# Performance work log

Hardware: AMD Instinct MI355X
Metric: run time of the kernel (lower is better)

The kernel has to match this reference:

```python
import jax, jax.numpy as jnp
import numpy as np

EMBED_DIM = 1024
NUM_HEADS = 16
HEAD_DIM = EMBED_DIM // NUM_HEADS
B, S = 2, 2048


def setup_inputs() -> dict:
    key = jax.random.key(0)
    ks = jax.random.split(key, 8)
    std = 1.0 / np.sqrt(EMBED_DIM)
    return {
        "xq": jax.random.normal(ks[0], (B, S, EMBED_DIM), jnp.float32),
        "xk": jax.random.normal(ks[1], (B, S, EMBED_DIM), jnp.float32),
        "xv": jax.random.normal(ks[2], (B, S, EMBED_DIM), jnp.float32),
        "Wq": jax.random.normal(ks[3], (EMBED_DIM, EMBED_DIM), jnp.float32) * std,
        "Wk": jax.random.normal(ks[4], (EMBED_DIM, EMBED_DIM), jnp.float32) * std,
        "Wv": jax.random.normal(ks[5], (EMBED_DIM, EMBED_DIM), jnp.float32) * std,
        "Wo": jax.random.normal(ks[6], (EMBED_DIM, EMBED_DIM), jnp.float32) * std,
        "bo": jnp.zeros((EMBED_DIM,), jnp.float32),
    }


def reference(xq, xk, xv, Wq, Wk, Wv, Wo, bo):
    # nn.Linear(x) = x @ W.T ; then view last dim into (heads, head_dim)
    def proj(x, W):
        y = jnp.einsum('bse,fe->bsf', x, W)
        return y.reshape(x.shape[0], x.shape[1], NUM_HEADS, HEAD_DIM)

    q = proj(xq, Wq)  # [b, m, h, f]
    k = proj(xk, Wk)  # [b, n, h, f]
    v = proj(xv, Wv)  # [b, n, h, f]

    scaling = 1.0 / np.sqrt(HEAD_DIM).astype(np.float32)
    dot = scaling * jnp.einsum('bmhf,bnhf->bhmn', q, k)  # [b, h, m, n]
    attn = jax.nn.softmax(dot, axis=-1)
    out = jnp.einsum('bhmn,bnhf->bmhf', attn, v)  # [b, m, h, f]

    Wo_hf = Wo.reshape(EMBED_DIM, NUM_HEADS, HEAD_DIM)
    return jnp.einsum('bmhf,ehf->bme', out, Wo_hf) + bo
```

## Files before the change

### kernel.cpp

```cpp
#include <hip/hip_runtime.h>
#include <math.h>


#define EMBED 1024
#define SEQ   2048
#define BATCH 2
#define NH    16
#define HD    64

typedef __attribute__((ext_vector_type(8))) short bf16x8;
typedef __attribute__((ext_vector_type(4))) short bf16x4;
typedef __attribute__((ext_vector_type(4))) float f32x4;
typedef __attribute__((ext_vector_type(4))) unsigned int u32x4;

#define QSCALE 0.18033688f

__device__ inline unsigned short f2bf(float f) {
  unsigned int u = __builtin_bit_cast(unsigned int, f);
  u += 0x7fffu + ((u >> 16) & 1u);
  return (unsigned short)(u >> 16);
}
__device__ inline float bf2f(unsigned short s) {
  unsigned int u = ((unsigned int)s) << 16;
  return __builtin_bit_cast(float, u);
}

__device__ inline unsigned packbf(float lo, float hi) {
  return __builtin_amdgcn_perm(__builtin_bit_cast(unsigned int, hi),
                               __builtin_bit_cast(unsigned int, lo),
                               0x07060302u);
}

__device__ inline void async_cp16(const void* g, void* l) {
  __builtin_amdgcn_global_load_lds(
      (const __attribute__((address_space(1))) unsigned int*)g,
      (__attribute__((address_space(3))) unsigned int*)l, 16, 0, 0);
}

__global__ void detect_kernel(const unsigned int* __restrict__ xq, int* __restrict__ flag) {
  __shared__ int cnt[256];
  int t = threadIdx.x;
  unsigned int w = xq[t];
  unsigned int e = (w >> 7) & 0xFFu;
  cnt[t] = (e >= 0x70u && e <= 0x8Fu) ? 1 : 0;
  __syncthreads();
  for (int s = 128; s > 0; s >>= 1) {
    if (t < s) cnt[t] += cnt[t + s];
    __syncthreads();
  }
  if (t == 0) *flag = (cnt[0] >= 160) ? 1 : 0;
}

struct PackPtrs {
  const void* src[7];
  unsigned short* dst[7];
};
__global__ __launch_bounds__(256) void pack_all(PackPtrs p, const int* __restrict__ flagp) {
  const bool isbf = (*flagp != 0);
  int ci = blockIdx.x * 256 + threadIdx.x;
  int t, rel;
  if (ci < 1572864) { t = ci / 524288; rel = ci - t * 524288; }
  else { int r = ci - 1572864; int w = r / 131072; t = 3 + w; rel = r - w * 131072; }
  size_t off = (size_t)rel * 8;
  unsigned short* d = p.dst[t] + off;
  if (isbf) {
    *(bf16x8*)d = *(const bf16x8*)((const unsigned short*)p.src[t] + off);
  } else {
    const float* s = (const float*)p.src[t] + off;
    f32x4 f0 = *(const f32x4*)s;
    f32x4 f1 = *(const f32x4*)(s + 4);
    bf16x8 v;
#pragma unroll
    for (int e = 0; e < 4; ++e) {
      v[e] = (short)f2bf(f0[e]);
      v[4 + e] = (short)f2bf(f1[e]);
    }
    *(bf16x8*)d = v;
  }
}

struct QkvArgs {
  const unsigned short* A[3];
  const unsigned short* W[3];
  unsigned short* out[3];
};
__global__ __launch_bounds__(256) void gemm_qkv(QkvArgs args) {
  __shared__ __align__(16) unsigned short smem[16640];

  const int z = blockIdx.z;
  const unsigned short* A = args.A[z];
  const unsigned short* Bw = args.W[z];
  unsigned short* out = args.out[z];

  const int tid = threadIdx.x, lane = tid & 63, wave = tid >> 6;
  const int wm = wave >> 1, wn = wave & 1;
  const int q = lane >> 4, c = lane & 15;
  const int m0 = blockIdx.x * 128, n0 = blockIdx.y * 128;

  f32x4 acc[4][4];
#pragma unroll
  for (int i = 0; i < 4; ++i)
#pragma unroll
    for (int j = 0; j < 4; ++j) acc[i][j] = (f32x4){0.f, 0.f, 0.f, 0.f};

  auto STAGE = [&](int buf, int k0) {
#pragma unroll
    for (int jj = 0; jj < 2; ++jj) {
      int ci = jj * 256 + tid;
      async_cp16(A + (size_t)(m0 + (ci >> 2)) * EMBED + k0 + (ci & 3) * 8,
                 (void*)(smem + buf * 8192 + (jj * 256 + wave * 64) * 8));
      async_cp16(Bw + (size_t)(n0 + (ci >> 2)) * EMBED + k0 + (ci & 3) * 8,
                 (void*)(smem + buf * 8192 + 4096 + (jj * 256 + wave * 64) * 8));
    }
  };

  STAGE(0, 0);
  __syncthreads();
  for (int kt = 0; kt < EMBED / 32; ++kt) {
    const int p = kt & 1;
    if (kt + 1 < EMBED / 32) STAGE(1 - p, (kt + 1) * 32);
    const unsigned short* Ab = smem + p * 8192;
    const unsigned short* Bb = smem + p * 8192 + 4096;

    bf16x8 af[4], bfr[4];
#pragma unroll
    for (int i = 0; i < 4; ++i)
      af[i] = *(const bf16x8*)(Ab + (wm * 64 + i * 16 + c) * 32 + q * 8);
#pragma unroll
    for (int j = 0; j < 4; ++j)
      bfr[j] = *(const bf16x8*)(Bb + (wn * 64 + j * 16 + c) * 32 + q * 8);
#pragma unroll
    for (int i = 0; i < 4; ++i)
#pragma unroll
      for (int j = 0; j < 4; ++j)
        acc[i][j] = __builtin_amdgcn_mfma_f32_16x16x32_bf16(af[i], bfr[j], acc[i][j], 0, 0, 0);
    __syncthreads();
  }

  if (z < 2) {
    const float sc = (z == 0) ? QSCALE : 1.0f;
#pragma unroll
    for (int i = 0; i < 4; ++i)
#pragma unroll
      for (int j = 0; j < 4; ++j)
#pragma unroll
        for (int r = 0; r < 4; ++r) {
          int m = m0 + wm * 64 + i * 16 + q * 4 + r;
          int col = n0 + wn * 64 + j * 16 + c;
          int b = m >> 11, s = m & 2047, h = col >> 6, d = col & 63;
          out[(size_t)((b * NH + h) * SEQ + s) * HD + d] = f2bf(acc[i][j][r] * sc);
        }
  } else {
    __syncthreads();
#pragma unroll
    for (int i = 0; i < 4; ++i)
#pragma unroll
      for (int j = 0; j < 4; ++j)
#pragma unroll
        for (int r = 0; r < 4; ++r)
          smem[(wm * 64 + i * 16 + q * 4 + r) * 130 + wn * 64 + j * 16 + c] =
              f2bf(acc[i][j][r]);
    __syncthreads();
    int n = tid >> 1;
    int sh = (tid & 1) * 64;
    int b = m0 >> 11, s0l = m0 & 2047;
    int h = blockIdx.y * 2 + (n >> 6), d = n & 63;
    unsigned short* dst = out + (size_t)((b * NH + h) * HD + d) * SEQ + s0l + sh;
#pragma unroll
    for (int g = 0; g < 8; ++g) {
      bf16x8 v;
#pragma unroll
      for (int e = 0; e < 8; ++e) v[e] = (short)smem[(sh + g * 8 + e) * 130 + n];
      *(bf16x8*)(dst + g * 8) = v;
    }
  }
}

__global__ __launch_bounds__(256) void gemm_out(
    const unsigned short* __restrict__ A,
    const unsigned short* __restrict__ Bw,
    const void* __restrict__ bias,
    void* __restrict__ out,
    const int* __restrict__ flagp)
{
  __shared__ __align__(16) unsigned short smem[16384];

  const int tid = threadIdx.x, lane = tid & 63, wave = tid >> 6;
  const int wm = wave >> 1, wn = wave & 1;
  const int q = lane >> 4, c = lane & 15;
  const int m0 = blockIdx.x * 128, n0 = blockIdx.y * 128;

  f32x4 acc[4][4];
#pragma unroll
  for (int i = 0; i < 4; ++i)
#pragma unroll
    for (int j = 0; j < 4; ++j) acc[i][j] = (f32x4){0.f, 0.f, 0.f, 0.f};

  auto STAGE = [&](int buf, int k0) {
#pragma unroll
    for (int jj = 0; jj < 2; ++jj) {
      int ci = jj * 256 + tid;
      async_cp16(A + (size_t)(m0 + (ci >> 2)) * EMBED + k0 + (ci & 3) * 8,
                 (void*)(smem + buf * 8192 + (jj * 256 + wave * 64) * 8));
      async_cp16(Bw + (size_t)(n0 + (ci >> 2)) * EMBED + k0 + (ci & 3) * 8,
                 (void*)(smem + buf * 8192 + 4096 + (jj * 256 + wave * 64) * 8));
    }
  };

  STAGE(0, 0);
  __syncthreads();
  for (int kt = 0; kt < EMBED / 32; ++kt) {
    const int p = kt & 1;
    if (kt + 1 < EMBED / 32) STAGE(1 - p, (kt + 1) * 32);
    const unsigned short* Ab = smem + p * 8192;
    const unsigned short* Bb = smem + p * 8192 + 4096;

    bf16x8 af[4], bfr[4];
#pragma unroll
    for (int i = 0; i < 4; ++i)
      af[i] = *(const bf16x8*)(Ab + (wm * 64 + i * 16 + c) * 32 + q * 8);
#pragma unroll
    for (int j = 0; j < 4; ++j)
      bfr[j] = *(const bf16x8*)(Bb + (wn * 64 + j * 16 + c) * 32 + q * 8);
#pragma unroll
    for (int i = 0; i < 4; ++i)
#pragma unroll
      for (int j = 0; j < 4; ++j)
        acc[i][j] = __builtin_amdgcn_mfma_f32_16x16x32_bf16(af[i], bfr[j], acc[i][j], 0, 0, 0);
    __syncthreads();
  }

  const bool isbf = (*flagp != 0);
#pragma unroll
  for (int i = 0; i < 4; ++i)
#pragma unroll
    for (int j = 0; j < 4; ++j)
#pragma unroll
      for (int r = 0; r < 4; ++r) {
        int m = m0 + wm * 64 + i * 16 + q * 4 + r;
        int col = n0 + wn * 64 + j * 16 + c;
        float v = acc[i][j][r];
        v += isbf ? bf2f(((const unsigned short*)bias)[col]) : ((const float*)bias)[col];
        if (isnan(v)) v = 777.0f;
        if (isbf) ((unsigned short*)out)[(size_t)m * EMBED + col] = f2bf(v);
        else      ((float*)out)[(size_t)m * EMBED + col] = v;
      }
}

__global__ __launch_bounds__(256) void attn_kernel(
    const unsigned short* __restrict__ Qb,
    const unsigned short* __restrict__ Kb,
    const unsigned short* __restrict__ Vtb,
    unsigned short* __restrict__ Ob)
{
  __shared__ __align__(16) unsigned short Kt[2][64][72];
  __shared__ __align__(16) unsigned short Vs[2][64][72];

  const int tid = threadIdx.x;
  const int lane = tid & 63;
  const int wave = tid >> 6;
  const int q = lane >> 4, c = lane & 15;
  const int b = blockIdx.z, h = blockIdx.y;
  const int q0 = blockIdx.x * 128 + wave * 32;

  const unsigned short* Qh = Qb + ((size_t)(b * NH + h) * SEQ) * HD;
  const unsigned short* Kh = Kb + ((size_t)(b * NH + h) * SEQ) * HD;
  const unsigned short* Vh = Vtb + ((size_t)(b * NH + h) * HD) * SEQ;

  bf16x8 qflA = *(const bf16x8*)(Qh + (q0 + c) * HD + q * 8);
  bf16x8 qfhA = *(const bf16x8*)(Qh + (q0 + c) * HD + 32 + q * 8);
  bf16x8 qflB = *(const bf16x8*)(Qh + (q0 + 16 + c) * HD + q * 8);
  bf16x8 qfhB = *(const bf16x8*)(Qh + (q0 + 16 + c) * HD + 32 + q * 8);

  f32x4 oA[4], oB[4];
#pragma unroll
  for (int t = 0; t < 4; ++t) { oA[t] = (f32x4){0.f,0.f,0.f,0.f}; oB[t] = (f32x4){0.f,0.f,0.f,0.f}; }
  f32x4 lA = (f32x4){0.f,0.f,0.f,0.f}, lB = (f32x4){0.f,0.f,0.f,0.f};

  bf16x8 ones;
#pragma unroll
  for (int e = 0; e < 8; ++e) ones[e] = (short)0x3F80;

  const int r0 = tid >> 3;
  const int t7 = tid & 7;
  const int ch0 = t7 * 8;
  const int u0 = 8 * (t7 >> 2) + 4 * (t7 & 1) + ((t7 >> 1) & 1);

  const bf16x8* pK0 = (const bf16x8*)(Kh + (size_t)r0 * HD + ch0);
  const bf16x8* pK1 = (const bf16x8*)(Kh + (size_t)(32 + r0) * HD + ch0);
  const bf16x8* pV0 = (const bf16x8*)(Vh + (size_t)r0 * SEQ + ch0);
  const bf16x8* pV1 = (const bf16x8*)(Vh + (size_t)(32 + r0) * SEQ + ch0);

  bf16x8 kr0, kr1, vr0, vr1;
  kr0 = *pK0; pK0 += (64 * HD) / 8;
  kr1 = *pK1; pK1 += (64 * HD) / 8;
  vr0 = *pV0; pV0 += 64 / 8;
  vr1 = *pV1; pV1 += 64 / 8;
  *(bf16x8*)(&Kt[0][r0][ch0]) = kr0;
  *(bf16x8*)(&Kt[0][32 + r0][ch0]) = kr1;
  {
    bf16x4 lo0 = __builtin_shufflevector(vr0, vr0, 0, 1, 2, 3);
    bf16x4 hi0 = __builtin_shufflevector(vr0, vr0, 4, 5, 6, 7);
    bf16x4 lo1 = __builtin_shufflevector(vr1, vr1, 0, 1, 2, 3);
    bf16x4 hi1 = __builtin_shufflevector(vr1, vr1, 4, 5, 6, 7);
    *(bf16x4*)(&Vs[0][r0][u0 * 4]) = lo0;
    *(bf16x4*)(&Vs[0][r0][u0 * 4 + 8]) = hi0;
    *(bf16x4*)(&Vs[0][32 + r0][u0 * 4]) = lo1;
    *(bf16x4*)(&Vs[0][32 + r0][u0 * 4 + 8]) = hi1;
  }

  for (int kt = 0; kt < SEQ / 64; ++kt) {
    const int p = kt & 1;
    __syncthreads();
    if (kt + 1 < SEQ / 64) {
      kr0 = *pK0; pK0 += (64 * HD) / 8;
      kr1 = *pK1; pK1 += (64 * HD) / 8;
      vr0 = *pV0; pV0 += 64 / 8;
      vr1 = *pV1; pV1 += 64 / 8;
    }

    bf16x8 kf0[4], kf1[4];
#pragma unroll
    for (int s = 0; s < 4; ++s) {
      kf0[s] = *(const bf16x8*)(&Kt[p][s * 16 + c][q * 8]);
      kf1[s] = *(const bf16x8*)(&Kt[p][s * 16 + c][32 + q * 8]);
    }

#pragma unroll
    for (int g = 0; g < 2; ++g) {
      u32x4 pa, pb;
#pragma unroll
      for (int s2 = 0; s2 < 2; ++s2) {
        const int s = g * 2 + s2;
        f32x4 zA = {0.f, 0.f, 0.f, 0.f};
        f32x4 zB = {0.f, 0.f, 0.f, 0.f};
        zA = __builtin_amdgcn_mfma_f32_16x16x32_bf16(kf0[s], qflA, zA, 0, 0, 0);
        zA = __builtin_amdgcn_mfma_f32_16x16x32_bf16(kf1[s], qfhA, zA, 0, 0, 0);
        zB = __builtin_amdgcn_mfma_f32_16x16x32_bf16(kf0[s], qflB, zB, 0, 0, 0);
        zB = __builtin_amdgcn_mfma_f32_16x16x32_bf16(kf1[s], qfhB, zB, 0, 0, 0);
        float a0 = __builtin_amdgcn_exp2f(zA[0]);
        float a1 = __builtin_amdgcn_exp2f(zA[1]);
        float a2 = __builtin_amdgcn_exp2f(zA[2]);
        float a3 = __builtin_amdgcn_exp2f(zA[3]);
        float b0 = __builtin_amdgcn_exp2f(zB[0]);
        float b1 = __builtin_amdgcn_exp2f(zB[1]);
        float b2 = __builtin_amdgcn_exp2f(zB[2]);
        float b3 = __builtin_amdgcn_exp2f(zB[3]);
        pa[s2 * 2]     = packbf(a0, a1);
        pa[s2 * 2 + 1] = packbf(a2, a3);
        pb[s2 * 2]     = packbf(b0, b1);
        pb[s2 * 2 + 1] = packbf(b2, b3);
      }
      bf16x8 pfA = __builtin_bit_cast(bf16x8, pa);
      bf16x8 pfB = __builtin_bit_cast(bf16x8, pb);
      __builtin_amdgcn_s_setprio(1);
      lA = __builtin_amdgcn_mfma_f32_16x16x32_bf16(pfA, ones, lA, 0, 0, 0);
      lB = __builtin_amdgcn_mfma_f32_16x16x32_bf16(pfB, ones, lB, 0, 0, 0);
#pragma unroll
      for (int t = 0; t < 4; ++t) {
        bf16x8 vf = *(const bf16x8*)(&Vs[p][t * 16 + c][(g * 4 + q) * 8]);
        oA[t] = __builtin_amdgcn_mfma_f32_16x16x32_bf16(pfA, vf, oA[t], 0, 0, 0);
        oB[t] = __builtin_amdgcn_mfma_f32_16x16x32_bf16(pfB, vf, oB[t], 0, 0, 0);
      }
      __builtin_amdgcn_s_setprio(0);
    }

    if (kt + 1 < SEQ / 64) {
      *(bf16x8*)(&Kt[1 - p][r0][ch0]) = kr0;
      *(bf16x8*)(&Kt[1 - p][32 + r0][ch0]) = kr1;
      bf16x4 lo0 = __builtin_shufflevector(vr0, vr0, 0, 1, 2, 3);
      bf16x4 hi0 = __builtin_shufflevector(vr0, vr0, 4, 5, 6, 7);
      bf16x4 lo1 = __builtin_shufflevector(vr1, vr1, 0, 1, 2, 3);
      bf16x4 hi1 = __builtin_shufflevector(vr1, vr1, 4, 5, 6, 7);
      *(bf16x4*)(&Vs[1 - p][r0][u0 * 4]) = lo0;
      *(bf16x4*)(&Vs[1 - p][r0][u0 * 4 + 8]) = hi0;
      *(bf16x4*)(&Vs[1 - p][32 + r0][u0 * 4]) = lo1;
      *(bf16x4*)(&Vs[1 - p][32 + r0][u0 * 4 + 8]) = hi1;
    }
  }

  float invA[4], invB[4];
#pragma unroll
  for (int r = 0; r < 4; ++r) { invA[r] = 1.0f / lA[r]; invB[r] = 1.0f / lB[r]; }
#pragma unroll
  for (int t = 0; t < 4; ++t)
#pragma unroll
    for (int r = 0; r < 4; ++r) {
      int col = h * HD + t * 16 + c;
      int srowA = q0 + q * 4 + r;
      float vA = oA[t][r] * invA[r];
      if (isnan(vA)) vA = 77.0f;
      Ob[((size_t)(b * SEQ + srowA)) * EMBED + col] = f2bf(vA);
      int srowB = q0 + 16 + q * 4 + r;
      float vB = oB[t][r] * invB[r];
      if (isnan(vB)) vB = 77.0f;
      Ob[((size_t)(b * SEQ + srowB)) * EMBED + col] = f2bf(vB);
    }
}

__device__ inline bf16x8 load8(const void* p, int idx, bool isbf) {
  if (isbf) return *(const bf16x8*)((const unsigned short*)p + idx);
  const float* f = (const float*)p + idx;
  bf16x8 r;
#pragma unroll
  for (int i = 0; i < 8; ++i) r[i] = (short)f2bf(f[i]);
  return r;
}
__global__ __launch_bounds__(256) void gemm_bt(
    const void* __restrict__ A, const void* __restrict__ Bw,
    const void* __restrict__ bias, void* __restrict__ out,
    const int* __restrict__ flagp, int mode, float scale)
{
  const bool isbf = (*flagp != 0);
  const bool a_isbf = isbf || (mode == 0);
  const int lane = threadIdx.x & 63;
  const int wave = threadIdx.x >> 6;
  const int tile = blockIdx.x * 4 + wave;
  const int mt = tile >> 4, nt = tile & 15;
  const int q = lane >> 4, c = lane & 15;
  const int m0 = mt * 16, n0 = nt * 64;

  f32x4 acc[4];
#pragma unroll
  for (int t = 0; t < 4; ++t) acc[t] = (f32x4){0.f, 0.f, 0.f, 0.f};

  for (int k0 = 0; k0 < EMBED; k0 += 32) {
    bf16x8 a = load8(A, (m0 + c) * EMBED + k0 + q * 8, a_isbf);
#pragma unroll
    for (int t = 0; t < 4; ++t) {
      bf16x8 b = load8(Bw, (n0 + t * 16 + c) * EMBED + k0 + q * 8, isbf);
      acc[t] = __builtin_amdgcn_mfma_f32_16x16x32_bf16(a, b, acc[t], 0, 0, 0);
    }
  }
#pragma unroll
  for (int t = 0; t < 4; ++t)
#pragma unroll
    for (int r = 0; r < 4; ++r) {
      float v = acc[t][r] * scale;
      int row = m0 + q * 4 + r, col = n0 + t * 16 + c;
      if (mode == 0) {
        v += isbf ? bf2f(((const unsigned short*)bias)[col]) : ((const float*)bias)[col];
        if (isbf) ((unsigned short*)out)[row * EMBED + col] = f2bf(v);
        else      ((float*)out)[row * EMBED + col] = v;
      } else {
        int b = row >> 11, s = row & 2047, h = col >> 6, d = col & 63;
        if (mode == 1) ((unsigned short*)out)[(((b * NH + h) * SEQ) + s) * HD + d] = f2bf(v);
        else           ((unsigned short*)out)[(((b * NH + h) * HD) + d) * SEQ + s] = f2bf(v);
      }
    }
}

extern "C" void kernel_launch(void* const* d_in, const int* in_sizes, int n_in,
                              void* d_out, int out_size, void* d_ws, size_t ws_size,
                              hipStream_t stream) {
  const void* xq = d_in[0]; const void* xk = d_in[1]; const void* xv = d_in[2];
  const void* Wq = d_in[3]; const void* Wk = d_in[4]; const void* Wv = d_in[5];
  const void* Wo = d_in[6]; const void* bo = d_in[7];

  const size_t NEL = (size_t)BATCH * SEQ * EMBED;
  const size_t WEL = (size_t)EMBED * EMBED;
  unsigned short* base = (unsigned short*)d_ws;

  unsigned short* Xq = base;
  unsigned short* Xk = Xq + NEL;
  unsigned short* Xv = Xk + NEL;
  unsigned short* Wqb = Xv + NEL;
  unsigned short* Wkb = Wqb + WEL;
  unsigned short* Wvb = Wkb + WEL;
  unsigned short* Wob = Wvb + WEL;
  unsigned short* Q  = Wob + WEL;
  unsigned short* K  = Q + NEL;
  unsigned short* Vt = K + NEL;
  unsigned short* AO = Xq;
  int* flagF = (int*)(Vt + NEL);
  size_t need = ((char*)(flagF + 16)) - (char*)d_ws;

  if (ws_size >= need) {
    detect_kernel<<<1, 256, 0, stream>>>((const unsigned int*)xq, flagF);
    PackPtrs pp;
    pp.src[0] = xq; pp.src[1] = xk; pp.src[2] = xv;
    pp.src[3] = Wq; pp.src[4] = Wk; pp.src[5] = Wv; pp.src[6] = Wo;
    pp.dst[0] = Xq; pp.dst[1] = Xk; pp.dst[2] = Xv;
    pp.dst[3] = Wqb; pp.dst[4] = Wkb; pp.dst[5] = Wvb; pp.dst[6] = Wob;
    pack_all<<<8192, 256, 0, stream>>>(pp, flagF);

    QkvArgs qa;
    qa.A[0] = Xq; qa.A[1] = Xk; qa.A[2] = Xv;
    qa.W[0] = Wqb; qa.W[1] = Wkb; qa.W[2] = Wvb;
    qa.out[0] = Q; qa.out[1] = K; qa.out[2] = Vt;
    gemm_qkv<<<dim3(32, 8, 3), 256, 0, stream>>>(qa);
    attn_kernel<<<dim3(SEQ / 128, NH, BATCH), 256, 0, stream>>>(Q, K, Vt, AO);
    gemm_out<<<dim3(32, 8), 256, 0, stream>>>(AO, Wob, bo, d_out, flagF);
  } else {
    unsigned short* Qf  = base;
    unsigned short* Kf  = Qf + NEL;
    unsigned short* Vtf = Kf + NEL;
    unsigned short* AOf = Vtf + NEL;
    int* flag = (int*)(AOf + NEL);
    detect_kernel<<<1, 256, 0, stream>>>((const unsigned int*)xq, flag);
    dim3 gblk(1024, 1, 1);
    gemm_bt<<<gblk, 256, 0, stream>>>(xq, Wq, nullptr, Qf, flag, 1, QSCALE);
    gemm_bt<<<gblk, 256, 0, stream>>>(xk, Wk, nullptr, Kf, flag, 1, 1.0f);
    gemm_bt<<<gblk, 256, 0, stream>>>(xv, Wv, nullptr, Vtf, flag, 2, 1.0f);
    attn_kernel<<<dim3(SEQ / 128, NH, BATCH), 256, 0, stream>>>(Qf, Kf, Vtf, AOf);
    gemm_bt<<<gblk, 256, 0, stream>>>(AOf, Wo, bo, d_out, flag, 0, 1.0f);
  }
}
```

Baseline: 230.5 us.

## Fuse fp32-to-bf16 conversion into GEMM loads and drop separate pack/detect kernels

Removes the standalone detect and pack_all kernels. The QKV and output GEMMs now load fp32 (or bf16) operands directly from global memory into registers, convert them to bf16, and write them to shared memory in a register-staged double-buffer pipeline. The dtype sniff is recomputed per block inside gemm_qkv. This avoids a full extra read/write pass over the inputs and weights plus two launches, but gives up async global-to-LDS copies and adds conversion ALU work and register pressure in the GEMM main loop.

```diff
diff --git a/kernel.cpp b/kernel.cpp
--- a/kernel.cpp
+++ b/kernel.cpp
@@ -29,12 +29,6 @@
   return __builtin_amdgcn_perm(__builtin_bit_cast(unsigned int, hi),
                                __builtin_bit_cast(unsigned int, lo),
                                0x07060302u);
-}
-
-__device__ inline void async_cp16(const void* g, void* l) {
-  __builtin_amdgcn_global_load_lds(
-      (const __attribute__((address_space(1))) unsigned int*)g,
-      (__attribute__((address_space(3))) unsigned int*)l, 16, 0, 0);
 }
 
 __global__ void detect_kernel(const unsigned int* __restrict__ xq, int* __restrict__ flag) {
@@ -51,45 +45,19 @@
   if (t == 0) *flag = (cnt[0] >= 160) ? 1 : 0;
 }
 
-struct PackPtrs {
-  const void* src[7];
-  unsigned short* dst[7];
-};
-__global__ __launch_bounds__(256) void pack_all(PackPtrs p, const int* __restrict__ flagp) {
-  const bool isbf = (*flagp != 0);
-  int ci = blockIdx.x * 256 + threadIdx.x;
-  int t, rel;
-  if (ci < 1572864) { t = ci / 524288; rel = ci - t * 524288; }
-  else { int r = ci - 1572864; int w = r / 131072; t = 3 + w; rel = r - w * 131072; }
-  size_t off = (size_t)rel * 8;
-  unsigned short* d = p.dst[t] + off;
-  if (isbf) {
-    *(bf16x8*)d = *(const bf16x8*)((const unsigned short*)p.src[t] + off);
-  } else {
-    const float* s = (const float*)p.src[t] + off;
-    f32x4 f0 = *(const f32x4*)s;
-    f32x4 f1 = *(const f32x4*)(s + 4);
-    bf16x8 v;
-#pragma unroll
-    for (int e = 0; e < 4; ++e) {
-      v[e] = (short)f2bf(f0[e]);
-      v[4 + e] = (short)f2bf(f1[e]);
-    }
-    *(bf16x8*)d = v;
-  }
-}
-
 struct QkvArgs {
-  const unsigned short* A[3];
-  const unsigned short* W[3];
+  const void* A[3];
+  const void* W[3];
   unsigned short* out[3];
+  const unsigned int* sniff;
+  int* flag;
 };
 __global__ __launch_bounds__(256) void gemm_qkv(QkvArgs args) {
   __shared__ __align__(16) unsigned short smem[16640];
 
   const int z = blockIdx.z;
-  const unsigned short* A = args.A[z];
-  const unsigned short* Bw = args.W[z];
+  const void* A = args.A[z];
+  const void* Bw = args.W[z];
   unsigned short* out = args.out[z];
 
   const int tid = threadIdx.x, lane = tid & 63, wave = tid >> 6;
@@ -97,30 +65,87 @@
   const int q = lane >> 4, c = lane & 15;
   const int m0 = blockIdx.x * 128, n0 = blockIdx.y * 128;
 
+  int* cnt = (int*)smem;
+  {
+    unsigned int w = args.sniff[tid];
+    unsigned int e = (w >> 7) & 0xFFu;
+    cnt[tid] = (e >= 0x70u && e <= 0x8Fu) ? 1 : 0;
+  }
+  __syncthreads();
+  for (int s = 128; s > 0; s >>= 1) {
+    if (tid < s) cnt[tid] += cnt[tid + s];
+    __syncthreads();
+  }
+  const bool isbf = (cnt[0] >= 160);
+  if (z == 0 && blockIdx.x == 0 && blockIdx.y == 0 && tid == 0)
+    *args.flag = isbf ? 1 : 0;
+  __syncthreads();
+
   f32x4 acc[4][4];
 #pragma unroll
   for (int i = 0; i < 4; ++i)
 #pragma unroll
     for (int j = 0; j < 4; ++j) acc[i][j] = (f32x4){0.f, 0.f, 0.f, 0.f};
 
-  auto STAGE = [&](int buf, int k0) {
-#pragma unroll
-    for (int jj = 0; jj < 2; ++jj) {
-      int ci = jj * 256 + tid;
-      async_cp16(A + (size_t)(m0 + (ci >> 2)) * EMBED + k0 + (ci & 3) * 8,
-                 (void*)(smem + buf * 8192 + (jj * 256 + wave * 64) * 8));
-      async_cp16(Bw + (size_t)(n0 + (ci >> 2)) * EMBED + k0 + (ci & 3) * 8,
-                 (void*)(smem + buf * 8192 + 4096 + (jj * 256 + wave * 64) * 8));
+  f32x4 rf[8];
+  bf16x8 rb[4];
+
+  auto LOAD = [&](int k0) {
+    if (isbf) {
+#pragma unroll
+      for (int j = 0; j < 2; ++j) {
+        int ci2 = j * 256 + tid;
+        rb[j]     = *(const bf16x8*)((const unsigned short*)A +
+                      (size_t)(m0 + (ci2 >> 2)) * EMBED + k0 + (ci2 & 3) * 8);
+        rb[2 + j] = *(const bf16x8*)((const unsigned short*)Bw +
+                      (size_t)(n0 + (ci2 >> 2)) * EMBED + k0 + (ci2 & 3) * 8);
+      }
+    } else {
+#pragma unroll
+      for (int j = 0; j < 2; ++j) {
+        int ci2 = j * 256 + tid;
+        const float* a = (const float*)A + (size_t)(m0 + (ci2 >> 2)) * EMBED + k0 + (ci2 & 3) * 8;
+        const float* b = (const float*)Bw + (size_t)(n0 + (ci2 >> 2)) * EMBED + k0 + (ci2 & 3) * 8;
+        rf[j * 2]     = *(const f32x4*)a;
+        rf[j * 2 + 1] = *(const f32x4*)(a + 4);
+        rf[4 + j * 2]     = *(const f32x4*)b;
+        rf[4 + j * 2 + 1] = *(const f32x4*)(b + 4);
+      }
     }
   };
-
-  STAGE(0, 0);
+  auto CVTWRITE = [&](int buf) {
+#pragma unroll
+    for (int j = 0; j < 2; ++j) {
+      int ci2 = j * 256 + tid;
+      unsigned short* dA = smem + buf * 8192 + ci2 * 8;
+      unsigned short* dB = smem + buf * 8192 + 4096 + ci2 * 8;
+      if (isbf) {
+        *(bf16x8*)dA = rb[j];
+        *(bf16x8*)dB = rb[2 + j];
+      } else {
+        bf16x8 va, vb;
+#pragma unroll
+        for (int e = 0; e < 4; ++e) {
+          va[e]     = (short)f2bf(rf[j * 2][e]);
+          va[4 + e] = (short)f2bf(rf[j * 2 + 1][e]);
+          vb[e]     = (short)f2bf(rf[4 + j * 2][e]);
+          vb[4 + e] = (short)f2bf(rf[4 + j * 2 + 1][e]);
+        }
+        *(bf16x8*)dA = va;
+        *(bf16x8*)dB = vb;
+      }
+    }
+  };
+
+  LOAD(0);
+  CVTWRITE(0);
+  LOAD(32);
   __syncthreads();
+
   for (int kt = 0; kt < EMBED / 32; ++kt) {
     const int p = kt & 1;
-    if (kt + 1 < EMBED / 32) STAGE(1 - p, (kt + 1) * 32);
     const unsigned short* Ab = smem + p * 8192;
-    const unsigned short* Bb = smem + p * 8192 + 4096;
+    const unsigned short* Bb = Ab + 4096;
 
     bf16x8 af[4], bfr[4];
 #pragma unroll
@@ -134,6 +159,9 @@
 #pragma unroll
       for (int j = 0; j < 4; ++j)
         acc[i][j] = __builtin_amdgcn_mfma_f32_16x16x32_bf16(af[i], bfr[j], acc[i][j], 0, 0, 0);
+
+    if (kt + 1 < EMBED / 32) CVTWRITE(1 - p);
+    if (kt + 2 < EMBED / 32) LOAD((kt + 2) * 32);
     __syncthreads();
   }
 
@@ -178,7 +206,7 @@
 
 __global__ __launch_bounds__(256) void gemm_out(
     const unsigned short* __restrict__ A,
-    const unsigned short* __restrict__ Bw,
+    const void* __restrict__ Bw,
     const void* __restrict__ bias,
     void* __restrict__ out,
     const int* __restrict__ flagp)
@@ -190,30 +218,63 @@
   const int q = lane >> 4, c = lane & 15;
   const int m0 = blockIdx.x * 128, n0 = blockIdx.y * 128;
 
+  const bool isbf = (*flagp != 0);
+
   f32x4 acc[4][4];
 #pragma unroll
   for (int i = 0; i < 4; ++i)
 #pragma unroll
     for (int j = 0; j < 4; ++j) acc[i][j] = (f32x4){0.f, 0.f, 0.f, 0.f};
 
-  auto STAGE = [&](int buf, int k0) {
-#pragma unroll
-    for (int jj = 0; jj < 2; ++jj) {
-      int ci = jj * 256 + tid;
-      async_cp16(A + (size_t)(m0 + (ci >> 2)) * EMBED + k0 + (ci & 3) * 8,
-                 (void*)(smem + buf * 8192 + (jj * 256 + wave * 64) * 8));
-      async_cp16(Bw + (size_t)(n0 + (ci >> 2)) * EMBED + k0 + (ci & 3) * 8,
-                 (void*)(smem + buf * 8192 + 4096 + (jj * 256 + wave * 64) * 8));
+  bf16x8 rbA[2];
+  f32x4 rfB[4];
+  bf16x8 rbB[2];
+
+  auto LOAD = [&](int k0) {
+#pragma unroll
+    for (int j = 0; j < 2; ++j) {
+      int ci2 = j * 256 + tid;
+      rbA[j] = *(const bf16x8*)(A + (size_t)(m0 + (ci2 >> 2)) * EMBED + k0 + (ci2 & 3) * 8);
+      if (isbf) {
+        rbB[j] = *(const bf16x8*)((const unsigned short*)Bw +
+                   (size_t)(n0 + (ci2 >> 2)) * EMBED + k0 + (ci2 & 3) * 8);
+      } else {
+        const float* b = (const float*)Bw + (size_t)(n0 + (ci2 >> 2)) * EMBED + k0 + (ci2 & 3) * 8;
+        rfB[j * 2]     = *(const f32x4*)b;
+        rfB[j * 2 + 1] = *(const f32x4*)(b + 4);
+      }
     }
   };
-
-  STAGE(0, 0);
+  auto CVTWRITE = [&](int buf) {
+#pragma unroll
+    for (int j = 0; j < 2; ++j) {
+      int ci2 = j * 256 + tid;
+      unsigned short* dA = smem + buf * 8192 + ci2 * 8;
+      unsigned short* dB = smem + buf * 8192 + 4096 + ci2 * 8;
+      *(bf16x8*)dA = rbA[j];
+      if (isbf) {
+        *(bf16x8*)dB = rbB[j];
+      } else {
+        bf16x8 vb;
+#pragma unroll
+        for (int e = 0; e < 4; ++e) {
+          vb[e]     = (short)f2bf(rfB[j * 2][e]);
+          vb[4 + e] = (short)f2bf(rfB[j * 2 + 1][e]);
+        }
+        *(bf16x8*)dB = vb;
+      }
+    }
+  };
+
+  LOAD(0);
+  CVTWRITE(0);
+  LOAD(32);
   __syncthreads();
+
   for (int kt = 0; kt < EMBED / 32; ++kt) {
     const int p = kt & 1;
-    if (kt + 1 < EMBED / 32) STAGE(1 - p, (kt + 1) * 32);
     const unsigned short* Ab = smem + p * 8192;
-    const unsigned short* Bb = smem + p * 8192 + 4096;
+    const unsigned short* Bb = Ab + 4096;
 
     bf16x8 af[4], bfr[4];
 #pragma unroll
@@ -227,10 +288,12 @@
 #pragma unroll
       for (int j = 0; j < 4; ++j)
         acc[i][j] = __builtin_amdgcn_mfma_f32_16x16x32_bf16(af[i], bfr[j], acc[i][j], 0, 0, 0);
-    __syncthreads();
-  }
-
-  const bool isbf = (*flagp != 0);
+
+    if (kt + 1 < EMBED / 32) CVTWRITE(1 - p);
+    if (kt + 2 < EMBED / 32) LOAD((kt + 2) * 32);
+    __syncthreads();
+  }
+
 #pragma unroll
   for (int i = 0; i < 4; ++i)
 #pragma unroll
@@ -458,39 +521,25 @@
   const void* Wo = d_in[6]; const void* bo = d_in[7];
 
   const size_t NEL = (size_t)BATCH * SEQ * EMBED;
-  const size_t WEL = (size_t)EMBED * EMBED;
   unsigned short* base = (unsigned short*)d_ws;
 
-  unsigned short* Xq = base;
-  unsigned short* Xk = Xq + NEL;
-  unsigned short* Xv = Xk + NEL;
-  unsigned short* Wqb = Xv + NEL;
-  unsigned short* Wkb = Wqb + WEL;
-  unsigned short* Wvb = Wkb + WEL;
-  unsigned short* Wob = Wvb + WEL;
-  unsigned short* Q  = Wob + WEL;
+  unsigned short* Q  = base;
   unsigned short* K  = Q + NEL;
   unsigned short* Vt = K + NEL;
-  unsigned short* AO = Xq;
-  int* flagF = (int*)(Vt + NEL);
+  unsigned short* AO = Vt + NEL;
+  int* flagF = (int*)(AO + NEL);
   size_t need = ((char*)(flagF + 16)) - (char*)d_ws;
 
   if (ws_size >= need) {
-    detect_kernel<<<1, 256, 0, stream>>>((const unsigned int*)xq, flagF);
-    PackPtrs pp;
-    pp.src[0] = xq; pp.src[1] = xk; pp.src[2] = xv;
-    pp.src[3] = Wq; pp.src[4] = Wk; pp.src[5] = Wv; pp.src[6] = Wo;
-    pp.dst[0] = Xq; pp.dst[1] = Xk; pp.dst[2] = Xv;
-    pp.dst[3] = Wqb; pp.dst[4] = Wkb; pp.dst[5] = Wvb; pp.dst[6] = Wob;
-    pack_all<<<8192, 256, 0, stream>>>(pp, flagF);
-
     QkvArgs qa;
-    qa.A[0] = Xq; qa.A[1] = Xk; qa.A[2] = Xv;
-    qa.W[0] = Wqb; qa.W[1] = Wkb; qa.W[2] = Wvb;
+    qa.A[0] = xq; qa.A[1] = xk; qa.A[2] = xv;
+    qa.W[0] = Wq; qa.W[1] = Wk; qa.W[2] = Wv;
     qa.out[0] = Q; qa.out[1] = K; qa.out[2] = Vt;
+    qa.sniff = (const unsigned int*)xq;
+    qa.flag = flagF;
     gemm_qkv<<<dim3(32, 8, 3), 256, 0, stream>>>(qa);
     attn_kernel<<<dim3(SEQ / 128, NH, BATCH), 256, 0, stream>>>(Q, K, Vt, AO);
-    gemm_out<<<dim3(32, 8), 256, 0, stream>>>(AO, Wob, bo, d_out, flagF);
+    gemm_out<<<dim3(32, 8), 256, 0, stream>>>(AO, Wo, bo, d_out, flagF);
   } else {
     unsigned short* Qf  = base;
     unsigned short* Kf  = Qf + NEL;
```

Result: slower. 300.9 us (+30.6%).
